# Kernel optimization log

Hardware: AMD Instinct MI355X
Metric: run time of the kernel (lower is better)

Reference implementation:

```python
import jax, jax.numpy as jnp
import numpy as np

B, NR_BOX, D = 512, 18, 2048
NR_OBJ = NR_BOX - 2
K = 3
NUM_CLASSES = 174
NUM_CAT = 321


def setup_inputs() -> dict:
    key = jax.random.key(0)
    k1, k2, k3, k4, k5, k6 = jax.random.split(key, 6)
    obj_fea = jax.random.normal(k1, (B, NR_BOX, D), dtype=jnp.float32)
    # cooccurrence: nonnegative, sparse-ish, first (pad) column zero as in the torch code
    cooc = jax.random.uniform(k2, (NUM_CLASSES, NUM_CAT), dtype=jnp.float32)
    mask = jax.random.uniform(k3, (NUM_CLASSES, NUM_CAT)) < 0.5
    cooc = jnp.where(mask, cooc, 0.0).at[:, 0].set(0.0)
    obj_indicator = jax.random.randint(k4, (B, NR_BOX), 0, 2).astype(jnp.int32)
    obj_category = jax.random.randint(k5, (B, NR_BOX), 0, NUM_CAT).astype(jnp.int32)
    labels = jax.random.randint(k6, (B,), 0, NUM_CLASSES).astype(jnp.int32)
    return {
        'obj_fea': obj_fea,
        'cooccurrence': cooc,
        'obj_indicator': obj_indicator,
        'obj_category': obj_category,
        'labels': labels,
    }


def reference(obj_fea, cooccurrence, obj_indicator, obj_category, labels):
    Bn, nr_box, d = obj_fea.shape
    nr_obj = nr_box - 2
    ind = obj_indicator[:, 2:]          # (B, nr_obj)
    cats = obj_category[:, 2:]          # (B, nr_obj)
    ori_comp = obj_fea.mean(axis=1)     # (B, d)
    objs = obj_fea[:, 2:]               # (B, nr_obj, d), hands dropped
    label_onehot = jax.nn.one_hot(labels, NUM_CLASSES, dtype=obj_fea.dtype)  # (B, C)

    # W[i, b, j] = cooccurrence[labels[i], cats[b, j]]  (candidate weights per sample i)
    cooc_lab = cooccurrence[labels]                 # (B, NUM_CAT)
    W = cooc_lab[:, cats]                           # (B, B, nr_obj)
    eye = jnp.eye(Bn, dtype=bool)
    W = jnp.where(eye[:, :, None], 0.0, W)          # exclude own video (cand_obj[i] = 0)
    Wf = W.reshape(Bn, Bn * nr_obj)

    # softmax(log w) over nonzero support == w / sum(w); sample via categorical on log-weights
    logits = jnp.where(Wf > 0, jnp.log(jnp.where(Wf > 0, Wf, 1.0)), -jnp.inf)
    has_cand = (Wf > 0).any(axis=1) & (ind != 0).any(axis=1)  # (B,)

    rng = jax.random.key(42)
    r1, r2, r3 = jax.random.split(rng, 3)
    sel = jax.random.categorical(r1, logits, shape=(K, Bn)).T   # (B, K) flat candidate ids
    batch_idx = sel // nr_obj
    box_idx = sel % nr_obj
    sel_fea = objs[batch_idx, box_idx]              # (B, K, d)
    sel_label = label_onehot[batch_idx]             # (B, K, C)

    lam = jax.random.uniform(r2, (Bn, 1, 1), dtype=obj_fea.dtype)  # Beta(1,1)==U(0,1), one per sample
    slots = jax.random.randint(r3, (Bn, K), 0, nr_obj)
    own_fea = jnp.take_along_axis(objs, slots[:, :, None], axis=1)  # (B, K, d)

    mixed_fea = own_fea * lam + sel_fea * (1.0 - lam)
    mixed_label = label_onehot[:, None, :] * lam + sel_label * (1.0 - lam)

    # fallback path: mean of own objects + own one-hot label, repeated K times
    fb_fea = jnp.broadcast_to(objs.mean(axis=1)[:, None, :], mixed_fea.shape)
    fb_label = jnp.broadcast_to(label_onehot[:, None, :], mixed_label.shape)
    m = has_cand[:, None, None]
    mix_fea = jnp.where(m, mixed_fea, fb_fea)
    mix_label = jnp.where(m, mixed_label, fb_label)
    return ori_comp, mix_fea, mix_label
```

## Files before the change

### kernel.cpp

```cpp
#include <hip/hip_runtime.h>
#include <stdint.h>
#include <math.h>

#define NBOX 18
#define BB 512
#define DD 2048
#define NOBJ 16
#define KK 3
#define NCLS 174
#define NCAT 321
#define NQ 4
#define QCAND 2048
#define TINYF 1.1754943508222875e-38f

__host__ __device__ __forceinline__ uint32_t rotl32(uint32_t x, int d) {
  return (x << d) | (x >> (32 - d));
}

__host__ __device__ __forceinline__ void threefry2x32(uint32_t k0, uint32_t k1,
                                                      uint32_t x0, uint32_t x1,
                                                      uint32_t& o0, uint32_t& o1) {
  uint32_t ks2 = k0 ^ k1 ^ 0x1BD11BDAu;
  x0 += k0; x1 += k1;
#define TFR(r) x0 += x1; x1 = rotl32(x1, r); x1 ^= x0;
#define R4A TFR(13) TFR(15) TFR(26) TFR(6)
#define R4B TFR(17) TFR(29) TFR(16) TFR(24)
  R4A x0 += k1;  x1 += ks2 + 1u;
  R4B x0 += ks2; x1 += k0 + 2u;
  R4A x0 += k0;  x1 += k1 + 3u;
  R4B x0 += k1;  x1 += ks2 + 4u;
  R4A x0 += ks2; x1 += k0 + 5u;
#undef R4A
#undef R4B
#undef TFR
  o0 = x0; o1 = x1;
}

__device__ __forceinline__ float bits_to_unit(uint32_t bits) {
  float f = __uint_as_float((bits >> 9) | 0x3f800000u);
  return f - 1.0f;
}

__global__ __launch_bounds__(256) void sample_kernel(
    const float* __restrict__ cooc, const int* __restrict__ obj_cat,
    const int* __restrict__ labels, uint32_t r1h, uint32_t r1l,
    unsigned long long* __restrict__ part, int* __restrict__ cnts) {
  const int gb = blockIdx.x;
  const int b = gb >> 2;
  const int q = gb & 3;
  const int tid = threadIdx.x;
  const int lane = tid & 63;
  const int wid = tid >> 6;

  __shared__ unsigned short jl[QCAND];
  __shared__ float wl[QCAND];
  __shared__ float pv[KK * 4];
  __shared__ int pj[KK * 4];
  __shared__ int wc[4];

  const int lab = labels[b];
  const float* crow = cooc + (size_t)lab * NCAT;
  const int seg = wid << 9;
  const int jbase = (q << 11) + seg;

  int cnt = 0;
#pragma unroll 1
  for (int c = 0; c < 8; ++c) {
    int j = jbase + (c << 6) + lane;
    int jb = j >> 4;
    float w = 0.0f;
    if (jb != b) w = crow[obj_cat[jb * NBOX + 2 + (j & 15)]];
    unsigned long long m = __ballot(w > 0.0f);
    if (w > 0.0f) {
      int rank = __popcll(m & ((1ull << lane) - 1ull));
      jl[seg + cnt + rank] = (unsigned short)j;
      wl[seg + cnt + rank] = w;
    }
    cnt += __popcll(m);
  }
  if (lane == 0) wc[wid] = cnt;

#pragma unroll 1
  for (int k = 0; k < KK; ++k) {
    uint32_t cbase = ((uint32_t)(k * BB + b)) << 13;
    float br = 0.0f;
    int bj = 0;
    for (int p = lane; p < cnt; p += 64) {
      uint32_t j = jl[seg + p];
      float w = wl[seg + p];
      uint32_t a0, a1;
      threefry2x32(r1h, r1l, 0u, cbase + j, a0, a1);
      float u = bits_to_unit(a0 ^ a1);
      if (u == 0.0f) u = TINYF;
      float t = -logf(u);
      if (w > br * t) { br = w / t; bj = (int)j; }
    }
#pragma unroll
    for (int mm = 1; mm < 64; mm <<= 1) {
      float ov = __shfl_xor(br, mm, 64);
      int oj = __shfl_xor(bj, mm, 64);
      if (ov > br || (ov == br && oj < bj)) { br = ov; bj = oj; }
    }
    if (lane == 0) { pv[k * 4 + wid] = br; pj[k * 4 + wid] = bj; }
  }
  __syncthreads();

  if (tid == 0) {
    cnts[gb] = wc[0] + wc[1] + wc[2] + wc[3];
#pragma unroll
    for (int k = 0; k < KK; ++k) {
      float bv = pv[k * 4]; int bj = pj[k * 4];
      for (int w4 = 1; w4 < 4; ++w4) {
        float vv = pv[k * 4 + w4]; int jj = pj[k * 4 + w4];
        if (vv > bv || (vv == bv && jj < bj)) { bv = vv; bj = jj; }
      }
      part[((size_t)b * KK + k) * NQ + q] =
          ((unsigned long long)__float_as_uint(bv) << 32) | (uint32_t)(8192 - bj);
    }
  }
}

__global__ __launch_bounds__(256) void finish_kernel(
    const float* __restrict__ obj_fea, const int* __restrict__ obj_ind,
    const int* __restrict__ labels,
    const unsigned long long* __restrict__ part, const int* __restrict__ cnts,
    uint32_t r2h, uint32_t r2l, uint32_t r3bh, uint32_t r3bl,
    float* __restrict__ ori, float* __restrict__ mixf, float* __restrict__ mixl) {
  const int bx = blockIdx.x;
  const int b = bx >> 1;
  const int h = bx & 1;
  const int tid = threadIdx.x;
  const int off = (h << 8) + tid;

  const float4* fea4 = (const float4*)obj_fea;
  const size_t rbase = (size_t)b * NBOX * 512 + off;

  float4 v0 = fea4[rbase];
  float4 v1 = fea4[rbase + 512];
  float4 S = make_float4(v0.x + v1.x, v0.y + v1.y, v0.z + v1.z, v0.w + v1.w);
#pragma unroll
  for (int r = 2; r < NBOX; ++r) {
    float4 a = fea4[rbase + (size_t)r * 512];
    S.x += a.x; S.y += a.y; S.z += a.z; S.w += a.w;
  }
  {
    const float is = 1.0f / 18.0f;
    float4 o = make_float4(S.x * is, S.y * is, S.z * is, S.w * is);
    ((float4*)ori)[(size_t)b * 512 + off] = o;
  }
  float4 S16 = make_float4(S.x - v0.x - v1.x, S.y - v0.y - v1.y,
                           S.z - v0.z - v1.z, S.w - v0.w - v1.w);

  __shared__ int s_sel[KK];
  __shared__ int s_slots[KK];
  __shared__ float s_lam;
  __shared__ int s_hc;
  if (tid < KK) {
    const int k = tid;
    unsigned long long best = part[((size_t)b * KK + k) * NQ];
#pragma unroll
    for (int q = 1; q < NQ; ++q) {
      unsigned long long p = part[((size_t)b * KK + k) * NQ + q];
      if (p > best) best = p;
    }
    s_sel[k] = 8192 - (int)(best & 0xFFFFFFFFull);
    uint32_t s0, s1;
    threefry2x32(r3bh, r3bl, 0u, (uint32_t)(b * KK + k), s0, s1);
    s_slots[k] = (int)((s0 ^ s1) & 15u);
  } else if (tid == 3) {
    int tot = cnts[b * NQ] + cnts[b * NQ + 1] + cnts[b * NQ + 2] + cnts[b * NQ + 3];
    int any = 0;
#pragma unroll
    for (int o = 0; o < NOBJ; ++o) any |= (obj_ind[b * NBOX + 2 + o] != 0);
    s_hc = (tot > 0) && any;
  } else if (tid == 4) {
    uint32_t c0, c1;
    threefry2x32(r2h, r2l, 0u, (uint32_t)b, c0, c1);
    s_lam = bits_to_unit(c0 ^ c1);
  }
  __syncthreads();

  const int hc = s_hc;
  const float l = s_lam, l1 = 1.0f - l;
  float4* mixf4 = (float4*)mixf;
  if (hc) {
#pragma unroll 1
    for (int k = 0; k < KK; ++k) {
      int s = s_sel[k];
      int bi = s >> 4, bo = s & 15, sl = s_slots[k];
      float4 a = fea4[((size_t)b * NBOX + 2 + sl) * 512 + off];
      float4 e = fea4[((size_t)bi * NBOX + 2 + bo) * 512 + off];
      float4 o;
      o.x = a.x * l + e.x * l1; o.y = a.y * l + e.y * l1;
      o.z = a.z * l + e.z * l1; o.w = a.w * l + e.w * l1;
      mixf4[((size_t)b * KK + k) * 512 + off] = o;
    }
  } else {
    const float is = 1.0f / 16.0f;
    float4 o = make_float4(S16.x * is, S16.y * is, S16.z * is, S16.w * is);
#pragma unroll
    for (int k = 0; k < KK; ++k) mixf4[((size_t)b * KK + k) * 512 + off] = o;
  }

  if (h == 0 && tid < NCLS) {
    int lb = labels[b];
#pragma unroll 1
    for (int k = 0; k < KK; ++k) {
      float val;
      if (hc) {
        int ls = labels[s_sel[k] >> 4];
        val = (tid == lb ? l : 0.0f) + (tid == ls ? l1 : 0.0f);
      } else {
        val = (tid == lb) ? 1.0f : 0.0f;
      }
      mixl[(size_t)(b * KK + k) * NCLS + tid] = val;
    }
  }
}

extern "C" void kernel_launch(void* const* d_in, const int* in_sizes, int n_in,
                              void* d_out, int out_size, void* d_ws, size_t ws_size,
                              hipStream_t stream) {
  (void)in_sizes; (void)n_in; (void)out_size; (void)ws_size;
  const float* obj_fea = (const float*)d_in[0];
  const float* cooc    = (const float*)d_in[1];
  const int* obj_ind   = (const int*)d_in[2];
  const int* obj_cat   = (const int*)d_in[3];
  const int* labels    = (const int*)d_in[4];

  float* out  = (float*)d_out;
  float* ori  = out;
  float* mixf = out + (size_t)BB * DD;
  float* mixl = mixf + (size_t)BB * KK * DD;

  unsigned long long* part = (unsigned long long*)d_ws;
  int* cnts = (int*)((char*)d_ws + (size_t)BB * KK * NQ * 8);

  uint32_t r1h, r1l, r2h, r2l, r3h, r3l;
  threefry2x32(0u, 42u, 0u, 0u, r1h, r1l);
  threefry2x32(0u, 42u, 0u, 1u, r2h, r2l);
  threefry2x32(0u, 42u, 0u, 2u, r3h, r3l);
  uint32_t r3bh, r3bl;
  threefry2x32(r3h, r3l, 0u, 1u, r3bh, r3bl);

  hipLaunchKernelGGL(sample_kernel, dim3(BB * NQ), dim3(256), 0, stream,
                     cooc, obj_cat, labels, r1h, r1l, part, cnts);
  hipLaunchKernelGGL(finish_kernel, dim3(BB * 2), dim3(256), 0, stream,
                     obj_fea, obj_ind, labels, part, cnts,
                     r2h, r2l, r3bh, r3bl, ori, mixf, mixl);
}
```

Before: 49.56 us.

## Move feature mean reduction into sampling kernel to overlap loads with RNG

```diff
diff --git a/kernel.cpp b/kernel.cpp
--- a/kernel.cpp
+++ b/kernel.cpp
@@ -41,10 +41,12 @@
   return f - 1.0f;
 }
 
-__global__ __launch_bounds__(256) void sample_kernel(
-    const float* __restrict__ cooc, const int* __restrict__ obj_cat,
-    const int* __restrict__ labels, uint32_t r1h, uint32_t r1l,
-    unsigned long long* __restrict__ part, int* __restrict__ cnts) {
+__global__ __launch_bounds__(256) void fused_sample_ori(
+    const float* __restrict__ obj_fea, const float* __restrict__ cooc,
+    const int* __restrict__ obj_cat, const int* __restrict__ labels,
+    uint32_t r1h, uint32_t r1l,
+    unsigned long long* __restrict__ part, int* __restrict__ cnts,
+    float* __restrict__ ori, float4* __restrict__ s16ws) {
   const int gb = blockIdx.x;
   const int b = gb >> 2;
   const int q = gb & 3;
@@ -57,12 +59,12 @@
   __shared__ float pv[KK * 4];
   __shared__ int pj[KK * 4];
   __shared__ int wc[4];
+  __shared__ float4 xch[128];
 
   const int lab = labels[b];
   const float* crow = cooc + (size_t)lab * NCAT;
   const int seg = wid << 9;
   const int jbase = (q << 11) + seg;
-
   int cnt = 0;
 #pragma unroll 1
   for (int c = 0; c < 8; ++c) {
@@ -80,6 +82,21 @@
   }
   if (lane == 0) wc[wid] = cnt;
 
+  const int col = tid & 127;
+  const int half = tid >> 7;
+  const float4* fea4 = (const float4*)obj_fea;
+  const size_t lbase = ((size_t)b * NBOX + half * 9) * 512 + (q << 7) + col;
+  float4 a0 = fea4[lbase];
+  float4 a1 = fea4[lbase + 512];
+  float4 a2 = fea4[lbase + 2 * 512];
+  float4 a3 = fea4[lbase + 3 * 512];
+  float4 a4 = fea4[lbase + 4 * 512];
+  float4 a5 = fea4[lbase + 5 * 512];
+  float4 a6 = fea4[lbase + 6 * 512];
+  float4 a7 = fea4[lbase + 7 * 512];
+  float4 a8 = fea4[lbase + 8 * 512];
+  __builtin_amdgcn_sched_barrier(0);
+
 #pragma unroll 1
   for (int k = 0; k < KK; ++k) {
     uint32_t cbase = ((uint32_t)(k * BB + b)) << 13;
@@ -88,9 +105,9 @@
     for (int p = lane; p < cnt; p += 64) {
       uint32_t j = jl[seg + p];
       float w = wl[seg + p];
-      uint32_t a0, a1;
-      threefry2x32(r1h, r1l, 0u, cbase + j, a0, a1);
-      float u = bits_to_unit(a0 ^ a1);
+      uint32_t t0, t1;
+      threefry2x32(r1h, r1l, 0u, cbase + j, t0, t1);
+      float u = bits_to_unit(t0 ^ t1);
       if (u == 0.0f) u = TINYF;
       float t = -logf(u);
       if (w > br * t) { br = w / t; bj = (int)j; }
@@ -118,38 +135,37 @@
           ((unsigned long long)__float_as_uint(bv) << 32) | (uint32_t)(8192 - bj);
     }
   }
-}
-
-__global__ __launch_bounds__(256) void finish_kernel(
+
+  float4 A;
+  A.x = a0.x + a1.x + a2.x + a3.x + a4.x + a5.x + a6.x + a7.x + a8.x;
+  A.y = a0.y + a1.y + a2.y + a3.y + a4.y + a5.y + a6.y + a7.y + a8.y;
+  A.z = a0.z + a1.z + a2.z + a3.z + a4.z + a5.z + a6.z + a7.z + a8.z;
+  A.w = a0.w + a1.w + a2.w + a3.w + a4.w + a5.w + a6.w + a7.w + a8.w;
+  if (half) xch[col] = A;
+  __syncthreads();
+  if (!half) {
+    float4 Bv = xch[col];
+    float4 S = make_float4(A.x + Bv.x, A.y + Bv.y, A.z + Bv.z, A.w + Bv.w);
+    const float is = 1.0f / 18.0f;
+    const size_t oidx = (size_t)b * 512 + (q << 7) + col;
+    ((float4*)ori)[oidx] = make_float4(S.x * is, S.y * is, S.z * is, S.w * is);
+    s16ws[oidx] = make_float4(S.x - a0.x - a1.x, S.y - a0.y - a1.y,
+                              S.z - a0.z - a1.z, S.w - a0.w - a1.w);
+  }
+}
+
+__global__ __launch_bounds__(256) void mix_kernel(
     const float* __restrict__ obj_fea, const int* __restrict__ obj_ind,
     const int* __restrict__ labels,
     const unsigned long long* __restrict__ part, const int* __restrict__ cnts,
+    const float4* __restrict__ s16ws,
     uint32_t r2h, uint32_t r2l, uint32_t r3bh, uint32_t r3bl,
-    float* __restrict__ ori, float* __restrict__ mixf, float* __restrict__ mixl) {
+    float* __restrict__ mixf, float* __restrict__ mixl) {
   const int bx = blockIdx.x;
   const int b = bx >> 1;
   const int h = bx & 1;
   const int tid = threadIdx.x;
   const int off = (h << 8) + tid;
-
-  const float4* fea4 = (const float4*)obj_fea;
-  const size_t rbase = (size_t)b * NBOX * 512 + off;
-
-  float4 v0 = fea4[rbase];
-  float4 v1 = fea4[rbase + 512];
-  float4 S = make_float4(v0.x + v1.x, v0.y + v1.y, v0.z + v1.z, v0.w + v1.w);
-#pragma unroll
-  for (int r = 2; r < NBOX; ++r) {
-    float4 a = fea4[rbase + (size_t)r * 512];
-    S.x += a.x; S.y += a.y; S.z += a.z; S.w += a.w;
-  }
-  {
-    const float is = 1.0f / 18.0f;
-    float4 o = make_float4(S.x * is, S.y * is, S.z * is, S.w * is);
-    ((float4*)ori)[(size_t)b * 512 + off] = o;
-  }
-  float4 S16 = make_float4(S.x - v0.x - v1.x, S.y - v0.y - v1.y,
-                           S.z - v0.z - v1.z, S.w - v0.w - v1.w);
 
   __shared__ int s_sel[KK];
   __shared__ int s_slots[KK];
@@ -159,8 +175,8 @@
     const int k = tid;
     unsigned long long best = part[((size_t)b * KK + k) * NQ];
 #pragma unroll
-    for (int q = 1; q < NQ; ++q) {
-      unsigned long long p = part[((size_t)b * KK + k) * NQ + q];
+    for (int qq = 1; qq < NQ; ++qq) {
+      unsigned long long p = part[((size_t)b * KK + k) * NQ + qq];
       if (p > best) best = p;
     }
     s_sel[k] = 8192 - (int)(best & 0xFFFFFFFFull);
@@ -182,6 +198,7 @@
 
   const int hc = s_hc;
   const float l = s_lam, l1 = 1.0f - l;
+  const float4* fea4 = (const float4*)obj_fea;
   float4* mixf4 = (float4*)mixf;
   if (hc) {
 #pragma unroll 1
@@ -196,8 +213,9 @@
       mixf4[((size_t)b * KK + k) * 512 + off] = o;
     }
   } else {
+    float4 s16 = s16ws[(size_t)b * 512 + off];
     const float is = 1.0f / 16.0f;
-    float4 o = make_float4(S16.x * is, S16.y * is, S16.z * is, S16.w * is);
+    float4 o = make_float4(s16.x * is, s16.y * is, s16.z * is, s16.w * is);
 #pragma unroll
     for (int k = 0; k < KK; ++k) mixf4[((size_t)b * KK + k) * 512 + off] = o;
   }
@@ -233,8 +251,10 @@
   float* mixf = out + (size_t)BB * DD;
   float* mixl = mixf + (size_t)BB * KK * DD;
 
-  unsigned long long* part = (unsigned long long*)d_ws;
-  int* cnts = (int*)((char*)d_ws + (size_t)BB * KK * NQ * 8);
+  char* ws = (char*)d_ws;
+  unsigned long long* part = (unsigned long long*)ws;
+  int* cnts = (int*)(ws + (size_t)BB * KK * NQ * 8);
+  float4* s16ws = (float4*)(ws + 64 * 1024);
 
   uint32_t r1h, r1l, r2h, r2l, r3h, r3l;
   threefry2x32(0u, 42u, 0u, 0u, r1h, r1l);
@@ -243,9 +263,10 @@
   uint32_t r3bh, r3bl;
   threefry2x32(r3h, r3l, 0u, 1u, r3bh, r3bl);
 
-  hipLaunchKernelGGL(sample_kernel, dim3(BB * NQ), dim3(256), 0, stream,
-                     cooc, obj_cat, labels, r1h, r1l, part, cnts);
-  hipLaunchKernelGGL(finish_kernel, dim3(BB * 2), dim3(256), 0, stream,
-                     obj_fea, obj_ind, labels, part, cnts,
-                     r2h, r2l, r3bh, r3bl, ori, mixf, mixl);
-}
+  hipLaunchKernelGGL(fused_sample_ori, dim3(BB * NQ), dim3(256), 0, stream,
+                     obj_fea, cooc, obj_cat, labels, r1h, r1l,
+                     part, cnts, ori, s16ws);
+  hipLaunchKernelGGL(mix_kernel, dim3(BB * 2), dim3(256), 0, stream,
+                     obj_fea, obj_ind, labels, part, cnts, s16ws,
+                     r2h, r2l, r3bh, r3bl, mixf, mixl);
+}
```

Result: faster. 43.03 us (-13.2%).

## Fuse K sampling passes, use log2 division-free argmax, drop block sync

Applied to the files above, without the earlier changes.

```diff
diff --git a/kernel.cpp b/kernel.cpp
--- a/kernel.cpp
+++ b/kernel.cpp
@@ -11,7 +11,7 @@
 #define NCAT 321
 #define NQ 4
 #define QCAND 2048
-#define TINYF 1.1754943508222875e-38f
+#define NPART 16
 
 __host__ __device__ __forceinline__ uint32_t rotl32(uint32_t x, int d) {
   return (x << d) | (x >> (32 - d));
@@ -54,9 +54,6 @@
 
   __shared__ unsigned short jl[QCAND];
   __shared__ float wl[QCAND];
-  __shared__ float pv[KK * 4];
-  __shared__ int pj[KK * 4];
-  __shared__ int wc[4];
 
   const int lab = labels[b];
   const float* crow = cooc + (size_t)lab * NCAT;
@@ -78,49 +75,54 @@
     }
     cnt += __popcll(m);
   }
-  if (lane == 0) wc[wid] = cnt;
-
-#pragma unroll 1
-  for (int k = 0; k < KK; ++k) {
-    uint32_t cbase = ((uint32_t)(k * BB + b)) << 13;
-    float br = 0.0f;
-    int bj = 0;
-    for (int p = lane; p < cnt; p += 64) {
-      uint32_t j = jl[seg + p];
-      float w = wl[seg + p];
-      uint32_t a0, a1;
-      threefry2x32(r1h, r1l, 0u, cbase + j, a0, a1);
-      float u = bits_to_unit(a0 ^ a1);
-      if (u == 0.0f) u = TINYF;
-      float t = -logf(u);
-      if (w > br * t) { br = w / t; bj = (int)j; }
-    }
-#pragma unroll
-    for (int mm = 1; mm < 64; mm <<= 1) {
-      float ov = __shfl_xor(br, mm, 64);
-      int oj = __shfl_xor(bj, mm, 64);
-      if (ov > br || (ov == br && oj < bj)) { br = ov; bj = oj; }
-    }
-    if (lane == 0) { pv[k * 4 + wid] = br; pj[k * 4 + wid] = bj; }
-  }
-  __syncthreads();
-
-  if (tid == 0) {
-    cnts[gb] = wc[0] + wc[1] + wc[2] + wc[3];
-#pragma unroll
-    for (int k = 0; k < KK; ++k) {
-      float bv = pv[k * 4]; int bj = pj[k * 4];
-      for (int w4 = 1; w4 < 4; ++w4) {
-        float vv = pv[k * 4 + w4]; int jj = pj[k * 4 + w4];
-        if (vv > bv || (vv == bv && jj < bj)) { bv = vv; bj = jj; }
-      }
-      part[((size_t)b * KK + k) * NQ + q] =
-          ((unsigned long long)__float_as_uint(bv) << 32) | (uint32_t)(8192 - bj);
-    }
-  }
-}
-
-__global__ __launch_bounds__(256) void finish_kernel(
+
+  const uint32_t cbase0 = ((uint32_t)b) << 13;
+  const uint32_t kstep = 1u << 22;
+  float bw0 = 0.f, bt0 = 1.f, bw1 = 0.f, bt1 = 1.f, bw2 = 0.f, bt2 = 1.f;
+  int bj0 = 0, bj1 = 0, bj2 = 0;
+#pragma unroll 1
+  for (int p = lane; p < cnt; p += 64) {
+    uint32_t j = jl[seg + p];
+    float w = wl[seg + p];
+    uint32_t cc = cbase0 + j;
+    uint32_t x0, x1, y0, y1, z0, z1;
+    threefry2x32(r1h, r1l, 0u, cc, x0, x1);
+    threefry2x32(r1h, r1l, 0u, cc + kstep, y0, y1);
+    threefry2x32(r1h, r1l, 0u, cc + 2u * kstep, z0, z1);
+    float t0 = -__log2f(fmaxf(bits_to_unit(x0 ^ x1), 1.1920929e-07f));
+    float t1 = -__log2f(fmaxf(bits_to_unit(y0 ^ y1), 1.1920929e-07f));
+    float t2 = -__log2f(fmaxf(bits_to_unit(z0 ^ z1), 1.1920929e-07f));
+    if (w * bt0 > bw0 * t0) { bw0 = w; bt0 = t0; bj0 = (int)j; }
+    if (w * bt1 > bw1 * t1) { bw1 = w; bt1 = t1; bj1 = (int)j; }
+    if (w * bt2 > bw2 * t2) { bw2 = w; bt2 = t2; bj2 = (int)j; }
+  }
+#pragma unroll
+  for (int mm = 1; mm < 64; mm <<= 1) {
+    float ow, ot; int oj;
+    ow = __shfl_xor(bw0, mm, 64); ot = __shfl_xor(bt0, mm, 64); oj = __shfl_xor(bj0, mm, 64);
+    { float l = ow * bt0, r = bw0 * ot;
+      if (l > r || (l == r && oj < bj0)) { bw0 = ow; bt0 = ot; bj0 = oj; } }
+    ow = __shfl_xor(bw1, mm, 64); ot = __shfl_xor(bt1, mm, 64); oj = __shfl_xor(bj1, mm, 64);
+    { float l = ow * bt1, r = bw1 * ot;
+      if (l > r || (l == r && oj < bj1)) { bw1 = ow; bt1 = ot; bj1 = oj; } }
+    ow = __shfl_xor(bw2, mm, 64); ot = __shfl_xor(bt2, mm, 64); oj = __shfl_xor(bj2, mm, 64);
+    { float l = ow * bt2, r = bw2 * ot;
+      if (l > r || (l == r && oj < bj2)) { bw2 = ow; bt2 = ot; bj2 = oj; } }
+  }
+  if (lane == 0) {
+    const int pw = q * 4 + wid;
+    const size_t pb = (size_t)b * KK * NPART;
+    part[pb + 0 * NPART + pw] =
+        ((unsigned long long)__float_as_uint(bw0 / bt0) << 32) | (uint32_t)(8192 - bj0);
+    part[pb + 1 * NPART + pw] =
+        ((unsigned long long)__float_as_uint(bw1 / bt1) << 32) | (uint32_t)(8192 - bj1);
+    part[pb + 2 * NPART + pw] =
+        ((unsigned long long)__float_as_uint(bw2 / bt2) << 32) | (uint32_t)(8192 - bj2);
+    cnts[b * NPART + pw] = cnt;
+  }
+}
+
+__global__ __launch_bounds__(256) void stream_mix_kernel(
     const float* __restrict__ obj_fea, const int* __restrict__ obj_ind,
     const int* __restrict__ labels,
     const unsigned long long* __restrict__ part, const int* __restrict__ cnts,
@@ -132,43 +134,28 @@
   const int tid = threadIdx.x;
   const int off = (h << 8) + tid;
 
-  const float4* fea4 = (const float4*)obj_fea;
-  const size_t rbase = (size_t)b * NBOX * 512 + off;
-
-  float4 v0 = fea4[rbase];
-  float4 v1 = fea4[rbase + 512];
-  float4 S = make_float4(v0.x + v1.x, v0.y + v1.y, v0.z + v1.z, v0.w + v1.w);
-#pragma unroll
-  for (int r = 2; r < NBOX; ++r) {
-    float4 a = fea4[rbase + (size_t)r * 512];
-    S.x += a.x; S.y += a.y; S.z += a.z; S.w += a.w;
-  }
-  {
-    const float is = 1.0f / 18.0f;
-    float4 o = make_float4(S.x * is, S.y * is, S.z * is, S.w * is);
-    ((float4*)ori)[(size_t)b * 512 + off] = o;
-  }
-  float4 S16 = make_float4(S.x - v0.x - v1.x, S.y - v0.y - v1.y,
-                           S.z - v0.z - v1.z, S.w - v0.w - v1.w);
-
   __shared__ int s_sel[KK];
   __shared__ int s_slots[KK];
   __shared__ float s_lam;
   __shared__ int s_hc;
+
   if (tid < KK) {
     const int k = tid;
-    unsigned long long best = part[((size_t)b * KK + k) * NQ];
-#pragma unroll
-    for (int q = 1; q < NQ; ++q) {
-      unsigned long long p = part[((size_t)b * KK + k) * NQ + q];
-      if (p > best) best = p;
+    const unsigned long long* pp = part + ((size_t)b * KK + k) * NPART;
+    unsigned long long best = pp[0];
+#pragma unroll
+    for (int p = 1; p < NPART; ++p) {
+      unsigned long long v = pp[p];
+      if (v > best) best = v;
     }
     s_sel[k] = 8192 - (int)(best & 0xFFFFFFFFull);
     uint32_t s0, s1;
     threefry2x32(r3bh, r3bl, 0u, (uint32_t)(b * KK + k), s0, s1);
     s_slots[k] = (int)((s0 ^ s1) & 15u);
   } else if (tid == 3) {
-    int tot = cnts[b * NQ] + cnts[b * NQ + 1] + cnts[b * NQ + 2] + cnts[b * NQ + 3];
+    int tot = 0;
+#pragma unroll
+    for (int p = 0; p < NPART; ++p) tot += cnts[b * NPART + p];
     int any = 0;
 #pragma unroll
     for (int o = 0; o < NOBJ; ++o) any |= (obj_ind[b * NBOX + 2 + o] != 0);
@@ -178,6 +165,24 @@
     threefry2x32(r2h, r2l, 0u, (uint32_t)b, c0, c1);
     s_lam = bits_to_unit(c0 ^ c1);
   }
+
+  const float4* fea4 = (const float4*)obj_fea;
+  const size_t rb = (size_t)b * NBOX * 512 + off;
+  float4 v0 = fea4[rb];
+  float4 v1 = fea4[rb + 512];
+  float4 S = make_float4(v0.x + v1.x, v0.y + v1.y, v0.z + v1.z, v0.w + v1.w);
+#pragma unroll
+  for (int r = 2; r < NBOX; ++r) {
+    float4 a = fea4[rb + (size_t)r * 512];
+    S.x += a.x; S.y += a.y; S.z += a.z; S.w += a.w;
+  }
+  {
+    const float is = 1.0f / 18.0f;
+    ((float4*)ori)[(size_t)b * 512 + off] =
+        make_float4(S.x * is, S.y * is, S.z * is, S.w * is);
+  }
+  float4 S16 = make_float4(S.x - v0.x - v1.x, S.y - v0.y - v1.y,
+                           S.z - v0.z - v1.z, S.w - v0.w - v1.w);
   __syncthreads();
 
   const int hc = s_hc;
@@ -233,8 +238,9 @@
   float* mixf = out + (size_t)BB * DD;
   float* mixl = mixf + (size_t)BB * KK * DD;
 
-  unsigned long long* part = (unsigned long long*)d_ws;
-  int* cnts = (int*)((char*)d_ws + (size_t)BB * KK * NQ * 8);
+  char* ws = (char*)d_ws;
+  unsigned long long* part = (unsigned long long*)ws;
+  int* cnts = (int*)(ws + (size_t)BB * KK * NPART * 8);
 
   uint32_t r1h, r1l, r2h, r2l, r3h, r3l;
   threefry2x32(0u, 42u, 0u, 0u, r1h, r1l);
@@ -245,7 +251,7 @@
 
   hipLaunchKernelGGL(sample_kernel, dim3(BB * NQ), dim3(256), 0, stream,
                      cooc, obj_cat, labels, r1h, r1l, part, cnts);
-  hipLaunchKernelGGL(finish_kernel, dim3(BB * 2), dim3(256), 0, stream,
+  hipLaunchKernelGGL(stream_mix_kernel, dim3(BB * 2), dim3(256), 0, stream,
                      obj_fea, obj_ind, labels, part, cnts,
                      r2h, r2l, r3bh, r3bl, ori, mixf, mixl);
 }
```

New measurement: 46.41 us. 1.07x faster.
